# Kernel optimization log

Hardware: AMD Instinct MI355X
Metric: run time of the kernel (lower is better)

Reference implementation:

```python
import jax, jax.numpy as jnp
import numpy as np

REPR_OUT = (16, 16, 16)   # multiplicities for l=0,1,2
STRIDE = 2                # GatedBlock stride with smooth_stride=True -> low-pass+stride after gate
PAD = 2                   # conv padding
C_IN = 72                 # 8*1 + 8*3 + 8*5
C_OUT_GATED = 176         # 144 fields + 32 gate scalars
KSIZE = 5


def conv3d(x, w, stride, padding):
    return jax.lax.conv_general_dilated(
        x, w, window_strides=(stride,) * 3,
        padding=[(padding, padding)] * 3,
        dimension_numbers=('NCDHW', 'OIDHW', 'NCDHW'))


def low_pass_filter(z, scale, stride):
    # gaussian blur (sigma from scale) applied depthwise, then strided -- as in se3cnn
    sigma = 0.5 * (scale ** 2 - 1) ** 0.5
    size = int(1 + 2 * 2.5 * sigma)
    if size % 2 == 0:
        size += 1
    r = np.arange(size) - size // 2
    g1 = np.exp(-r.astype(np.float64) ** 2 / (2 * sigma ** 2))
    g = g1[:, None, None] * g1[None, :, None] * g1[None, None, :]
    g = (g / g.sum()).astype(np.float32)
    B, C = z.shape[0], z.shape[1]
    zz = z.reshape(B * C, 1, *z.shape[2:])
    out = conv3d(zz, jnp.asarray(g)[None, None], stride, size // 2)
    return out.reshape(B, C, *out.shape[2:])


def gate(y, scalar_bias, gate_bias):
    # y: [B, 176, X, Y, Z]; split into 144 field channels + 32 gate scalars
    size_out = sum(mul * (2 * n + 1) for n, mul in enumerate(REPR_OUT))
    B, _, nx, ny, nz = y.shape
    g = jax.nn.sigmoid(y[:, size_out:] + gate_bias[None, :, None, None, None])
    fields = []
    begin_y, begin_g = 0, 0
    for n, mul in enumerate(REPR_OUT):
        if mul == 0:
            continue
        dim = 2 * n + 1
        fy = y[:, begin_y:begin_y + mul * dim]
        if n == 0:
            # scalar fields: bias + relu (ScalarActivation)
            fields.append(jax.nn.relu(fy + scalar_bias[None, :, None, None, None]))
        else:
            fg = g[:, begin_g:begin_g + mul]
            begin_g += mul
            f = fy.reshape(B, mul, dim, nx, ny, nz) * fg[:, :, None]  # broadcast gate over 2l+1
            fields.append(f.reshape(B, mul * dim, nx, ny, nz))
        begin_y += mul * dim
    return jnp.concatenate(fields, axis=1)  # [B, 144, X, Y, Z]


def setup_inputs() -> dict:
    key = jax.random.key(0)
    k1, k2, k3, k4 = jax.random.split(key, 4)
    fan_in = C_IN * KSIZE ** 3
    x = jax.random.normal(k1, (4, C_IN, 32, 32, 32), dtype=jnp.float32)
    W = jax.random.normal(k2, (C_OUT_GATED, C_IN, KSIZE, KSIZE, KSIZE), dtype=jnp.float32) / np.sqrt(fan_in)
    scalar_bias = jax.random.normal(k3, (REPR_OUT[0],), dtype=jnp.float32) * 0.1
    gate_bias = jax.random.normal(k4, (sum(REPR_OUT[1:]),), dtype=jnp.float32) * 0.1
    return {'x': x, 'W': W, 'scalar_bias': scalar_bias, 'gate_bias': gate_bias}


def reference(x, W, scalar_bias, gate_bias):
    y = conv3d(x, W, 1, PAD)                 # SE3 conv at stride 1 (smooth_stride)
    z = gate(y, scalar_bias, gate_bias)      # per-irrep gated nonlinearity
    z = low_pass_filter(z, STRIDE, STRIDE)   # gaussian low-pass + stride 2
    return z
```

## Files before the change

### kernel.cpp

```cpp
#include <hip/hip_runtime.h>
#include <cstdint>
#include <cstddef>

typedef short short8 __attribute__((ext_vector_type(8)));
typedef float floatx4 __attribute__((ext_vector_type(4)));
typedef unsigned short u16;

__device__ __forceinline__ u16 f2bf(float f) {
    unsigned u = __float_as_uint(f);
    u += 0x7FFFu + ((u >> 16) & 1u);
    return (u16)(u >> 16);
}
__device__ __forceinline__ float bf2f(u16 h) {
    return __uint_as_float(((unsigned)h) << 16);
}

__device__ __forceinline__ void gload_lds16(const u16* g, u16* l) {
    __builtin_amdgcn_global_load_lds(
        (const __attribute__((address_space(1))) void*)g,
        (__attribute__((address_space(3))) void*)l, 16, 0, 0);
}

__global__ __launch_bounds__(256) void k_transpose_x(const float* __restrict__ x,
                                                     u16* __restrict__ xt) {
    __shared__ float tile[72 * 33];
    const int bx = blockIdx.x;
    const int tid = threadIdx.x;
    const int b = bx >> 10, d = (bx >> 5) & 31, h = bx & 31;
    const float* src = x + (size_t)b * 72 * 32768 + d * 1024 + h * 32;
    for (int e = tid; e < 2304; e += 256) {
        int ci = e >> 5, w = e & 31;
        tile[ci * 33 + w] = src[(size_t)ci * 32768 + w];
    }
    __syncthreads();
    u16* dst = xt + (size_t)bx * 2304;
    for (int e = tid; e < 2304; e += 256) {
        int w = e / 72, ci = e - w * 72;
        dst[e] = f2bf(tile[ci * 33 + w]);
    }
}

__global__ __launch_bounds__(256) void k_prep_w(const float* __restrict__ W,
                                                u16* __restrict__ wt) {
    const int gid = blockIdx.x * 256 + threadIdx.x;
    const int frag = gid >> 6, lane = gid & 63;
    const int nb = frag % 11;
    int t = frag / 11;
    const int kb = t % 12;
    t = t / 12;
    const int kh = t % 5, kd = t / 5;
    const int n = lane & 15, q8 = (lane >> 4) * 8;
    const int co = nb * 16 + n;
    u16 v[8] __attribute__((aligned(16)));
    #pragma unroll
    for (int j = 0; j < 8; ++j) {
        int k = kb * 32 + q8 + j;
        u16 r = 0;
        if (k < 360) {
            int kw = k / 72, ci = k - kw * 72;
            r = f2bf(W[((size_t)co * 72 + ci) * 125 + kd * 25 + kh * 5 + kw]);
        }
        v[j] = r;
    }
    *(uint4*)(wt + (size_t)gid * 8) = *(const uint4*)v;
}

#define LP 2624
#define MFMA_BF16 __builtin_amdgcn_mfma_f32_16x16x32_bf16

#define STAGE_PAIR(s0_) do {                                                       \
    _Pragma("unroll")                                                              \
    for (int cc = 0; cc < 3; ++cc) {                                               \
        const int c_  = wv + cc * 8;                                               \
        const int st_ = (s0_) + (c_ >= 11 ? 1 : 0);                                \
        const int nb_ = (c_ >= 11) ? (c_ - 11) : c_;                               \
        if (c_ < 22 && st_ < 60)                                                   \
            gload_lds16(wt_kd + (size_t)st_ * 5632 + nb_ * 512 + lane * 8,         \
                        sB + (st_ & 3) * 5632 + nb_ * 512);                        \
    }                                                                              \
} while (0)

#define CSTEP(aoff_, buf_) do {                                                    \
    const u16* ap_ = sxA + (aoff_);                                                \
    short8 A0_ = *(const short8*)(ap_);                                            \
    short8 A1_ = *(const short8*)(ap_ + 1152);                                     \
    short8 A2_ = *(const short8*)(ap_ + LP);                                       \
    short8 A3_ = *(const short8*)(ap_ + LP + 1152);                                \
    const u16* bb_ = sB + (buf_) * 5632 + lane * 8;                                \
    _Pragma("unroll")                                                              \
    for (int j = 0; j < 11; ++j) {                                                 \
        short8 bv = *(const short8*)(bb_ + j * 512);                               \
        acc[0][j] = MFMA_BF16(A0_, bv, acc[0][j], 0, 0, 0);                        \
        acc[1][j] = MFMA_BF16(A1_, bv, acc[1][j], 0, 0, 0);                        \
        acc[2][j] = MFMA_BF16(A2_, bv, acc[2][j], 0, 0, 0);                        \
        acc[3][j] = MFMA_BF16(A3_, bv, acc[3][j], 0, 0, 0);                        \
    }                                                                              \
} while (0)

__global__ __launch_bounds__(512, 2) void k_conv(const u16* __restrict__ xt,
                                                 const u16* __restrict__ wt,
                                                 const float* __restrict__ scalar_bias,
                                                 const float* __restrict__ gate_bias,
                                                 u16* __restrict__ zt) {
    __shared__ __align__(16) u16 sx[20 * LP];
    __shared__ __align__(16) u16 sB[4 * 5632];
    const int bx = blockIdx.x;
    const int ht = bx & 1, d = (bx >> 1) & 31, b = bx >> 6;
    const int h0 = ht * 16;
    const int tid = threadIdx.x, lane = tid & 63, wv = tid >> 6;
    const int c15 = lane & 15, q = lane >> 4;

    floatx4 acc[4][11];
    #pragma unroll
    for (int i = 0; i < 4; ++i) {
        #pragma unroll
        for (int j = 0; j < 11; ++j) acc[i][j] = (floatx4){0.f, 0.f, 0.f, 0.f};
    }

    const int laneA = c15 * 72 + q * 8;
    const u16* sxA = &sx[2 * wv * LP + laneA];

    for (int kd = 0; kd < 5; ++kd) {
        const int dp = d + kd - 2;
        if (dp < 0 || dp >= 32) continue;
        const u16* wt_kd = wt + (size_t)kd * 5 * 67584;

        __syncthreads();
        const u16* srcbase = xt + (size_t)((b * 32 + dp) * 32) * 2304;
        for (int idx = tid; idx < 20 * 328; idx += 512) {
            int r = idx / 328, c = idx - r * 328;
            int hp = h0 + r - 2;
            uint4 val = make_uint4(0u, 0u, 0u, 0u);
            if (hp >= 0 && hp < 32 && c >= 18 && c < 306)
                val = *(const uint4*)(srcbase + (size_t)hp * 2304 + (c * 8 - 144));
            *(uint4*)(&sx[r * LP + c * 8]) = val;
        }
        STAGE_PAIR(0);
        __syncthreads();

        int kh = 0, kb = 0;
        #pragma unroll 1
        for (int kp = 0; kp < 60; kp += 2) {
            if (kp) __syncthreads();
            STAGE_PAIR(kp + 2);
            const int aoff = kh * LP + kb * 32;
            CSTEP(aoff,      kp & 3);
            CSTEP(aoff + 32, (kp + 1) & 3);
            kb += 2;
            if (kb == 12) { kb = 0; ++kh; }
        }
    }

    const float sb = scalar_bias[c15];
    int   slA[9];
    float gbA[9];
    #pragma unroll
    for (int nb = 1; nb <= 8; ++nb) {
        int idx = (nb - 1) * 16 + c15;
        int mul = (nb <= 3) ? (idx / 3) : (16 + (idx - 48) / 5);
        slA[nb] = (lane & 48) | (mul & 15);
        gbA[nb] = gate_bias[mul];
    }
    #pragma unroll
    for (int mi = 0; mi < 4; ++mi) {
        const int hl = 2 * wv + (mi >> 1);
        const int wh = mi & 1;
        const size_t zrow0 = (size_t)((b * 32 + d) * 32 + (h0 + hl)) * 32;
        #pragma unroll
        for (int r = 0; r < 4; ++r) {
            const int w = wh * 16 + q * 4 + r;
            u16* zp = zt + (zrow0 + w) * 144;
            zp[c15] = f2bf(fmaxf(acc[mi][0][r] + sb, 0.f));
            const float g9v  = acc[mi][9][r];
            const float g10v = acc[mi][10][r];
            #pragma unroll
            for (int nb = 1; nb <= 8; ++nb) {
                float ys = __shfl((nb <= 3) ? g9v : g10v, slA[nb], 64);
                float g  = 1.f / (1.f + __expf(-(ys + gbA[nb])));
                zp[nb * 16 + c15] = f2bf(acc[mi][nb][r] * g);
            }
        }
    }
}

__global__ __launch_bounds__(256) void k_lowpass(const u16* __restrict__ zt,
                                                 float* __restrict__ out) {
    const int gid = blockIdx.x * 256 + threadIdx.x;
    const int row = gid / 288;
    const int it  = gid - row * 288;
    const int c8 = it >> 4, ow = it & 15;
    const int oh = row & 15, od = (row >> 4) & 15, b = row >> 8;
    const float lw[5] = {0.03208210f, 0.23705644f, 0.46172277f, 0.23705644f, 0.03208210f};
    float a[8];
    #pragma unroll
    for (int j = 0; j < 8; ++j) a[j] = 0.f;
    for (int kd = 0; kd < 5; ++kd) {
        const int dz = 2 * od + kd - 2;
        if (dz < 0 || dz >= 32) continue;
        for (int kh = 0; kh < 5; ++kh) {
            const int hz = 2 * oh + kh - 2;
            if (hz < 0 || hz >= 32) continue;
            const float whd = lw[kd] * lw[kh];
            const u16* base = zt + (size_t)((b * 32 + dz) * 32 + hz) * 32 * 144 + c8 * 8;
            #pragma unroll
            for (int kw = 0; kw < 5; ++kw) {
                const int wz = 2 * ow + kw - 2;
                if (wz < 0 || wz >= 32) continue;
                const float wt3 = whd * lw[kw];
                u16 v[8] __attribute__((aligned(16)));
                *(uint4*)v = *(const uint4*)(base + (size_t)wz * 144);
                #pragma unroll
                for (int j = 0; j < 8; ++j) a[j] += wt3 * bf2f(v[j]);
            }
        }
    }
    const int c0 = c8 * 8;
    float* op = out + ((size_t)b * 144 + c0) * 4096 + od * 256 + oh * 16 + ow;
    #pragma unroll
    for (int j = 0; j < 8; ++j) op[(size_t)j * 4096] = a[j];
}

extern "C" void kernel_launch(void* const* d_in, const int* in_sizes, int n_in,
                              void* d_out, int out_size, void* d_ws, size_t ws_size,
                              hipStream_t stream) {
    const float* x  = (const float*)d_in[0];
    const float* W  = (const float*)d_in[1];
    const float* sb = (const float*)d_in[2];
    const float* gb = (const float*)d_in[3];
    float* out = (float*)d_out;

    char* ws = (char*)d_ws;
    u16* xt = (u16*)(ws);
    u16* wt = (u16*)(ws + 18874368);
    u16* zt = (u16*)(ws + 22253568);

    hipLaunchKernelGGL(k_transpose_x, dim3(4096), dim3(256), 0, stream, x, xt);
    hipLaunchKernelGGL(k_prep_w,      dim3(825),  dim3(256), 0, stream, W, wt);
    hipLaunchKernelGGL(k_conv,        dim3(256),  dim3(512), 0, stream, xt, wt, sb, gb, zt);
    hipLaunchKernelGGL(k_lowpass,     dim3(1152), dim3(256), 0, stream, zt, out);
}
```

Before: 494.0 us.

## Load conv A-fragments from global into registers, stage weights in larger halves

Drops the LDS staging of the padded input slab. Each wave now loads its A fragments straight from global memory into two ping-pong register sets, prefetching the next k-step while MFMAs run on the current one. Weights are staged six k-steps at a time into two large LDS buffers, which cuts block barriers from 30 to 10 per kd slice. Block indices are also remapped to improve L2 locality. The trade-off is that input rows are no longer shared through LDS, so global/L2 traffic rises and global-load latency must be hidden by the register prefetch.

New measurement: 958.7 us. 1.94x slower.

```diff
diff --git a/kernel.cpp b/kernel.cpp
--- a/kernel.cpp
+++ b/kernel.cpp
@@ -65,35 +65,47 @@
     *(uint4*)(wt + (size_t)gid * 8) = *(const uint4*)v;
 }
 
-#define LP 2624
 #define MFMA_BF16 __builtin_amdgcn_mfma_f32_16x16x32_bf16
 
-#define STAGE_PAIR(s0_) do {                                                       \
-    _Pragma("unroll")                                                              \
-    for (int cc = 0; cc < 3; ++cc) {                                               \
-        const int c_  = wv + cc * 8;                                               \
-        const int st_ = (s0_) + (c_ >= 11 ? 1 : 0);                                \
-        const int nb_ = (c_ >= 11) ? (c_ - 11) : c_;                               \
-        if (c_ < 22 && st_ < 60)                                                   \
-            gload_lds16(wt_kd + (size_t)st_ * 5632 + nb_ * 512 + lane * 8,         \
-                        sB + (st_ & 3) * 5632 + nb_ * 512);                        \
-    }                                                                              \
+#define LOADA(A_, kh_, kb_) do {                                                   \
+    const int hp_ = h0 + 2 * wv + (kh_) - 2;                                       \
+    const int e_  = laneE + (kb_) * 32;                                            \
+    const bool r0_ = (unsigned)hp_ < 32u;                                          \
+    const bool r1_ = (unsigned)(hp_ + 1) < 32u;                                    \
+    const bool c0_ = (unsigned)e_ < 2304u;                                         \
+    const bool c1_ = (unsigned)(e_ + 1152) < 2304u;                                \
+    const u16* rp_ = xslice + (size_t)hp_ * 2304 + e_;                             \
+    short8 t0_ = (short8)0, t1_ = (short8)0, t2_ = (short8)0, t3_ = (short8)0;     \
+    if (r0_ && c0_) t0_ = *(const short8*)(rp_);                                   \
+    if (r0_ && c1_) t1_ = *(const short8*)(rp_ + 1152);                            \
+    if (r1_ && c0_) t2_ = *(const short8*)(rp_ + 2304);                            \
+    if (r1_ && c1_) t3_ = *(const short8*)(rp_ + 2304 + 1152);                     \
+    A_##0 = t0_; A_##1 = t1_; A_##2 = t2_; A_##3 = t3_;                            \
 } while (0)
 
-#define CSTEP(aoff_, buf_) do {                                                    \
-    const u16* ap_ = sxA + (aoff_);                                                \
-    short8 A0_ = *(const short8*)(ap_);                                            \
-    short8 A1_ = *(const short8*)(ap_ + 1152);                                     \
-    short8 A2_ = *(const short8*)(ap_ + LP);                                       \
-    short8 A3_ = *(const short8*)(ap_ + LP + 1152);                                \
-    const u16* bb_ = sB + (buf_) * 5632 + lane * 8;                                \
+#define CSTEPB(A_, bofs_) do {                                                     \
+    const u16* bb_ = bbB + (bofs_);                                                \
     _Pragma("unroll")                                                              \
     for (int j = 0; j < 11; ++j) {                                                 \
         short8 bv = *(const short8*)(bb_ + j * 512);                               \
-        acc[0][j] = MFMA_BF16(A0_, bv, acc[0][j], 0, 0, 0);                        \
-        acc[1][j] = MFMA_BF16(A1_, bv, acc[1][j], 0, 0, 0);                        \
-        acc[2][j] = MFMA_BF16(A2_, bv, acc[2][j], 0, 0, 0);                        \
-        acc[3][j] = MFMA_BF16(A3_, bv, acc[3][j], 0, 0, 0);                        \
+        acc[0][j] = MFMA_BF16(A_##0, bv, acc[0][j], 0, 0, 0);                      \
+        acc[1][j] = MFMA_BF16(A_##1, bv, acc[1][j], 0, 0, 0);                      \
+        acc[2][j] = MFMA_BF16(A_##2, bv, acc[2][j], 0, 0, 0);                      \
+        acc[3][j] = MFMA_BF16(A_##3, bv, acc[3][j], 0, 0, 0);                      \
+    }                                                                              \
+} while (0)
+
+#define STAGE_HALF(H_) do {                                                        \
+    const int kk0_ = (H_) * 6;                                                     \
+    u16* db_ = sB + ((H_) & 1) * 33792;                                            \
+    _Pragma("unroll")                                                              \
+    for (int cc = 0; cc < 9; ++cc) {                                               \
+        const int c_ = wv + cc * 8;                                                \
+        if (c_ < 66) {                                                             \
+            const int kbl_ = c_ / 11, nb_ = c_ - kbl_ * 11;                        \
+            gload_lds16(wt_kd + (size_t)(kk0_ + kbl_) * 5632 + nb_ * 512 + lane * 8, \
+                        db_ + kbl_ * 5632 + nb_ * 512);                            \
+        }                                                                          \
     }                                                                              \
 } while (0)
 
@@ -102,10 +114,10 @@
                                                  const float* __restrict__ scalar_bias,
                                                  const float* __restrict__ gate_bias,
                                                  u16* __restrict__ zt) {
-    __shared__ __align__(16) u16 sx[20 * LP];
-    __shared__ __align__(16) u16 sB[4 * 5632];
+    __shared__ __align__(16) u16 sB[2 * 33792];
     const int bx = blockIdx.x;
-    const int ht = bx & 1, d = (bx >> 1) & 31, b = bx >> 6;
+    const int logical = (bx & 7) * 32 + (bx >> 3);
+    const int ht = logical & 1, d = (logical >> 1) & 31, b = logical >> 6;
     const int h0 = ht * 16;
     const int tid = threadIdx.x, lane = tid & 63, wv = tid >> 6;
     const int c15 = lane & 15, q = lane >> 4;
@@ -117,37 +129,32 @@
         for (int j = 0; j < 11; ++j) acc[i][j] = (floatx4){0.f, 0.f, 0.f, 0.f};
     }
 
-    const int laneA = c15 * 72 + q * 8;
-    const u16* sxA = &sx[2 * wv * LP + laneA];
+    const int laneE = c15 * 72 + q * 8 - 144;
+    short8 XA0, XA1, XA2, XA3, YA0, YA1, YA2, YA3;
 
     for (int kd = 0; kd < 5; ++kd) {
         const int dp = d + kd - 2;
         if (dp < 0 || dp >= 32) continue;
-        const u16* wt_kd = wt + (size_t)kd * 5 * 67584;
-
+        const u16* wt_kd  = wt + (size_t)kd * 5 * 67584;
+        const u16* xslice = xt + (size_t)((b * 32 + dp) * 32) * 2304;
+
+        LOADA(XA, 0, 0);
+        STAGE_HALF(0);
         __syncthreads();
-        const u16* srcbase = xt + (size_t)((b * 32 + dp) * 32) * 2304;
-        for (int idx = tid; idx < 20 * 328; idx += 512) {
-            int r = idx / 328, c = idx - r * 328;
-            int hp = h0 + r - 2;
-            uint4 val = make_uint4(0u, 0u, 0u, 0u);
-            if (hp >= 0 && hp < 32 && c >= 18 && c < 306)
-                val = *(const uint4*)(srcbase + (size_t)hp * 2304 + (c * 8 - 144));
-            *(uint4*)(&sx[r * LP + c * 8]) = val;
-        }
-        STAGE_PAIR(0);
-        __syncthreads();
-
-        int kh = 0, kb = 0;
+
         #pragma unroll 1
-        for (int kp = 0; kp < 60; kp += 2) {
-            if (kp) __syncthreads();
-            STAGE_PAIR(kp + 2);
-            const int aoff = kh * LP + kb * 32;
-            CSTEP(aoff,      kp & 3);
-            CSTEP(aoff + 32, (kp + 1) & 3);
-            kb += 2;
-            if (kb == 12) { kb = 0; ++kh; }
+        for (int H = 0; H < 10; ++H) {
+            if (H < 9) STAGE_HALF(H + 1);
+            const int kh  = H >> 1,        kb0  = (H & 1) * 6;
+            const int khn = (H + 1) >> 1,  kb0n = ((H + 1) & 1) * 6;
+            const u16* bbB = sB + (H & 1) * 33792 + lane * 8;
+            LOADA(YA, kh, kb0 + 1);  CSTEPB(XA, 0 * 5632);
+            LOADA(XA, kh, kb0 + 2);  CSTEPB(YA, 1 * 5632);
+            LOADA(YA, kh, kb0 + 3);  CSTEPB(XA, 2 * 5632);
+            LOADA(XA, kh, kb0 + 4);  CSTEPB(YA, 3 * 5632);
+            LOADA(YA, kh, kb0 + 5);  CSTEPB(XA, 4 * 5632);
+            LOADA(XA, khn, kb0n);    CSTEPB(YA, 5 * 5632);
+            __syncthreads();
         }
     }
 
```

## Deepen weight staging pipeline to three stages with per-step barriers and block swizzle

Applied to the files above, without the earlier changes.

Restructures the inner K loop of the conv kernel so weight tiles are prefetched three steps ahead into a 4-slot LDS ring. A manual vmcnt wait plus raw s_barrier replaces the paired __syncthreads, and all B fragments are loaded into registers before the MFMAs, which run at raised priority. It also swizzles block indices and spreads the per-stage loads across waves, with redundant loads of chunks 8-10. The aim is to hide global-to-LDS latency and improve cache locality, at the cost of more barriers per K step and higher register pressure.

Result: slower. 538.6 us (+9.0%).

```diff
diff --git a/kernel.cpp b/kernel.cpp
--- a/kernel.cpp
+++ b/kernel.cpp
@@ -68,33 +68,41 @@
 #define LP 2624
 #define MFMA_BF16 __builtin_amdgcn_mfma_f32_16x16x32_bf16
 
-#define STAGE_PAIR(s0_) do {                                                       \
-    _Pragma("unroll")                                                              \
-    for (int cc = 0; cc < 3; ++cc) {                                               \
-        const int c_  = wv + cc * 8;                                               \
-        const int st_ = (s0_) + (c_ >= 11 ? 1 : 0);                                \
-        const int nb_ = (c_ >= 11) ? (c_ - 11) : c_;                               \
-        if (c_ < 22 && st_ < 60)                                                   \
-            gload_lds16(wt_kd + (size_t)st_ * 5632 + nb_ * 512 + lane * 8,         \
-                        sB + (st_ & 3) * 5632 + nb_ * 512);                        \
-    }                                                                              \
+#define STAGE(kk_, slot_) do {                                                     \
+    const int kks_ = (kk_) < 60 ? (kk_) : 0;       \
+    const u16* gs_ = wt_kd + (size_t)kks_ * 5632 + lane * 8;                       \
+    u16* ds_ = sB + (slot_) * 5632;                                                \
+    gload_lds16(gs_ + wv * 512, ds_ + wv * 512);                                   \
+    gload_lds16(gs_ + c2w * 512, ds_ + c2w * 512);                                 \
 } while (0)
 
-#define CSTEP(aoff_, buf_) do {                                                    \
-    const u16* ap_ = sxA + (aoff_);                                                \
+#define PHASE(slot_) do {                                                          \
+    asm volatile("s_waitcnt vmcnt(4)" ::: "memory");                               \
+    __builtin_amdgcn_s_barrier();                                                  \
+    __builtin_amdgcn_sched_barrier(0);                                             \
+    const u16* ap_ = sx + (2 * wv + kh) * LP + laneA + kb * 32;                    \
     short8 A0_ = *(const short8*)(ap_);                                            \
     short8 A1_ = *(const short8*)(ap_ + 1152);                                     \
     short8 A2_ = *(const short8*)(ap_ + LP);                                       \
     short8 A3_ = *(const short8*)(ap_ + LP + 1152);                                \
-    const u16* bb_ = sB + (buf_) * 5632 + lane * 8;                                \
+    const u16* bb_ = sB + (slot_) * 5632 + lane * 8;                               \
+    short8 bv_[11];                                                                \
+    _Pragma("unroll")                                                              \
+    for (int j = 0; j < 11; ++j) bv_[j] = *(const short8*)(bb_ + j * 512);         \
+    STAGE(kk + 3, ((slot_) + 3) & 3);                                              \
+    __builtin_amdgcn_s_setprio(1);                                                 \
     _Pragma("unroll")                                                              \
     for (int j = 0; j < 11; ++j) {                                                 \
-        short8 bv = *(const short8*)(bb_ + j * 512);                               \
-        acc[0][j] = MFMA_BF16(A0_, bv, acc[0][j], 0, 0, 0);                        \
-        acc[1][j] = MFMA_BF16(A1_, bv, acc[1][j], 0, 0, 0);                        \
-        acc[2][j] = MFMA_BF16(A2_, bv, acc[2][j], 0, 0, 0);                        \
-        acc[3][j] = MFMA_BF16(A3_, bv, acc[3][j], 0, 0, 0);                        \
+        acc[0][j] = MFMA_BF16(A0_, bv_[j], acc[0][j], 0, 0, 0);                    \
+        acc[1][j] = MFMA_BF16(A1_, bv_[j], acc[1][j], 0, 0, 0);                    \
+        acc[2][j] = MFMA_BF16(A2_, bv_[j], acc[2][j], 0, 0, 0);                    \
+        acc[3][j] = MFMA_BF16(A3_, bv_[j], acc[3][j], 0, 0, 0);                    \
     }                                                                              \
+    __builtin_amdgcn_s_setprio(0);                                                 \
+    __builtin_amdgcn_sched_barrier(0);                                             \
+    __builtin_amdgcn_s_barrier();                                                  \
+    ++kk;                                                                          \
+    if (++kb == 12) { kb = 0; ++kh; }                                              \
 } while (0)
 
 __global__ __launch_bounds__(512, 2) void k_conv(const u16* __restrict__ xt,
@@ -105,10 +113,12 @@
     __shared__ __align__(16) u16 sx[20 * LP];
     __shared__ __align__(16) u16 sB[4 * 5632];
     const int bx = blockIdx.x;
-    const int ht = bx & 1, d = (bx >> 1) & 31, b = bx >> 6;
+    const int swz = (bx & 7) * 32 + (bx >> 3);
+    const int ht = swz & 1, d = (swz >> 1) & 31, b = swz >> 6;
     const int h0 = ht * 16;
     const int tid = threadIdx.x, lane = tid & 63, wv = tid >> 6;
     const int c15 = lane & 15, q = lane >> 4;
+    const int c2w = 8 + wv % 3;
 
     floatx4 acc[4][11];
     #pragma unroll
@@ -118,7 +128,6 @@
     }
 
     const int laneA = c15 * 72 + q * 8;
-    const u16* sxA = &sx[2 * wv * LP + laneA];
 
     for (int kd = 0; kd < 5; ++kd) {
         const int dp = d + kd - 2;
@@ -135,19 +144,18 @@
                 val = *(const uint4*)(srcbase + (size_t)hp * 2304 + (c * 8 - 144));
             *(uint4*)(&sx[r * LP + c * 8]) = val;
         }
-        STAGE_PAIR(0);
+        STAGE(0, 0);
+        STAGE(1, 1);
+        STAGE(2, 2);
         __syncthreads();
 
-        int kh = 0, kb = 0;
+        int kk = 0, kh = 0, kb = 0;
         #pragma unroll 1
-        for (int kp = 0; kp < 60; kp += 2) {
-            if (kp) __syncthreads();
-            STAGE_PAIR(kp + 2);
-            const int aoff = kh * LP + kb * 32;
-            CSTEP(aoff,      kp & 3);
-            CSTEP(aoff + 32, (kp + 1) & 3);
-            kb += 2;
-            if (kb == 12) { kb = 0; ++kh; }
+        for (int kp = 0; kp < 15; ++kp) {
+            PHASE(0);
+            PHASE(1);
+            PHASE(2);
+            PHASE(3);
         }
     }
 
```

## Split 3D low-pass into separable HW and D passes, swizzle conv block order

Applied to the files above, without the earlier changes.

Replaces the fused 125-tap low-pass with two passes. The first applies the 25-tap H/W filter per depth slice into an fp32 scratch buffer reused from the xt region. The second applies the 5-tap depth filter and writes output rows contiguously. The aim is to cut redundant bf16 gather loads, at the cost of an extra launch and a round trip through the intermediate buffer. The conv block index is also swizzled so that concurrently running blocks cover different batches and depths, which changes L2 locality.

New measurement: 532.6 us. +7.8%, slower.

```diff
diff --git a/kernel.cpp b/kernel.cpp
--- a/kernel.cpp
+++ b/kernel.cpp
@@ -105,7 +105,8 @@
     __shared__ __align__(16) u16 sx[20 * LP];
     __shared__ __align__(16) u16 sB[4 * 5632];
     const int bx = blockIdx.x;
-    const int ht = bx & 1, d = (bx >> 1) & 31, b = bx >> 6;
+    const int swz = (bx & 7) * 32 + (bx >> 3);
+    const int ht = swz & 1, d = (swz >> 1) & 31, b = swz >> 6;
     const int h0 = ht * 16;
     const int tid = threadIdx.x, lane = tid & 63, wv = tid >> 6;
     const int c15 = lane & 15, q = lane >> 4;
@@ -183,41 +184,63 @@
     }
 }
 
-__global__ __launch_bounds__(256) void k_lowpass(const u16* __restrict__ zt,
-                                                 float* __restrict__ out) {
+__global__ __launch_bounds__(256) void k_lowpass_wh(const u16* __restrict__ zt,
+                                                    float* __restrict__ tmp) {
     const int gid = blockIdx.x * 256 + threadIdx.x;
-    const int row = gid / 288;
-    const int it  = gid - row * 288;
-    const int c8 = it >> 4, ow = it & 15;
-    const int oh = row & 15, od = (row >> 4) & 15, b = row >> 8;
+    const int c8 = gid % 18;
+    int r = gid / 18;
+    const int ow = r & 15; r >>= 4;
+    const int oh = r & 15; r >>= 4;
+    const int d = r & 31;
+    const int b = r >> 5;
     const float lw[5] = {0.03208210f, 0.23705644f, 0.46172277f, 0.23705644f, 0.03208210f};
     float a[8];
     #pragma unroll
     for (int j = 0; j < 8; ++j) a[j] = 0.f;
+    const u16* zb = zt + (size_t)((b * 32 + d) * 32) * 32 * 144 + c8 * 8;
+    for (int kh = 0; kh < 5; ++kh) {
+        const int hz = 2 * oh + kh - 2;
+        if (hz < 0 || hz >= 32) continue;
+        const u16* rowp = zb + (size_t)hz * 32 * 144;
+        #pragma unroll
+        for (int kw = 0; kw < 5; ++kw) {
+            const int wz = 2 * ow + kw - 2;
+            if (wz < 0 || wz >= 32) continue;
+            const float wt2 = lw[kh] * lw[kw];
+            u16 v[8] __attribute__((aligned(16)));
+            *(uint4*)v = *(const uint4*)(rowp + (size_t)wz * 144);
+            #pragma unroll
+            for (int j = 0; j < 8; ++j) a[j] += wt2 * bf2f(v[j]);
+        }
+    }
+    float* tp = tmp + (size_t)(((b * 32 + d) * 16 + oh) * 16 + ow) * 144 + c8 * 8;
+    *(float4*)(tp)     = make_float4(a[0], a[1], a[2], a[3]);
+    *(float4*)(tp + 4) = make_float4(a[4], a[5], a[6], a[7]);
+}
+
+__global__ __launch_bounds__(256) void k_lowpass_d(const float* __restrict__ tmp,
+                                                   float* __restrict__ out) {
+    const int gid = blockIdx.x * 256 + threadIdx.x;
+    const int oh = gid & 15;
+    int r = gid >> 4;
+    const int od = r & 15; r >>= 4;
+    const int c = r % 144;
+    const int b = r / 144;
+    const float lw[5] = {0.03208210f, 0.23705644f, 0.46172277f, 0.23705644f, 0.03208210f};
+    float a[16];
+    #pragma unroll
+    for (int j = 0; j < 16; ++j) a[j] = 0.f;
     for (int kd = 0; kd < 5; ++kd) {
         const int dz = 2 * od + kd - 2;
         if (dz < 0 || dz >= 32) continue;
-        for (int kh = 0; kh < 5; ++kh) {
-            const int hz = 2 * oh + kh - 2;
-            if (hz < 0 || hz >= 32) continue;
-            const float whd = lw[kd] * lw[kh];
-            const u16* base = zt + (size_t)((b * 32 + dz) * 32 + hz) * 32 * 144 + c8 * 8;
-            #pragma unroll
-            for (int kw = 0; kw < 5; ++kw) {
-                const int wz = 2 * ow + kw - 2;
-                if (wz < 0 || wz >= 32) continue;
-                const float wt3 = whd * lw[kw];
-                u16 v[8] __attribute__((aligned(16)));
-                *(uint4*)v = *(const uint4*)(base + (size_t)wz * 144);
-                #pragma unroll
-                for (int j = 0; j < 8; ++j) a[j] += wt3 * bf2f(v[j]);
-            }
-        }
-    }
-    const int c0 = c8 * 8;
-    float* op = out + ((size_t)b * 144 + c0) * 4096 + od * 256 + oh * 16 + ow;
-    #pragma unroll
-    for (int j = 0; j < 8; ++j) op[(size_t)j * 4096] = a[j];
+        const float w = lw[kd];
+        const float* base = tmp + (size_t)(((b * 32 + dz) * 16 + oh) * 16) * 144 + c;
+        #pragma unroll
+        for (int ow = 0; ow < 16; ++ow) a[ow] += w * base[(size_t)ow * 144];
+    }
+    float* op = out + ((size_t)(b * 144 + c) * 4096) + od * 256 + oh * 16;
+    #pragma unroll
+    for (int ow = 0; ow < 16; ++ow) op[ow] = a[ow];
 }
 
 extern "C" void kernel_launch(void* const* d_in, const int* in_sizes, int n_in,
@@ -233,9 +256,11 @@
     u16* xt = (u16*)(ws);
     u16* wt = (u16*)(ws + 18874368);
     u16* zt = (u16*)(ws + 22253568);
+    float* tmp = (float*)(ws);
 
     hipLaunchKernelGGL(k_transpose_x, dim3(4096), dim3(256), 0, stream, x, xt);
     hipLaunchKernelGGL(k_prep_w,      dim3(825),  dim3(256), 0, stream, W, wt);
     hipLaunchKernelGGL(k_conv,        dim3(256),  dim3(512), 0, stream, xt, wt, sb, gb, zt);
-    hipLaunchKernelGGL(k_lowpass,     dim3(1152), dim3(256), 0, stream, zt, out);
-}
+    hipLaunchKernelGGL(k_lowpass_wh,  dim3(2304), dim3(256), 0, stream, zt, tmp);
+    hipLaunchKernelGGL(k_lowpass_d,   dim3(576),  dim3(256), 0, stream, tmp, out);
+}
```
